# Kernel optimization log

Hardware: AMD Instinct MI355X
Metric: run time of the kernel (lower is better)

## Reference

```python
import jax, jax.numpy as jnp
import numpy as np

N_NODES = 500000
N_EDGES = 8000000
IN_DIM = 128
H1, H2, OUT = 32, 16, 2


def gcn_conv(x, W, b, src, dst, n):
    # PyG GCNConv: linear transform, add self-loops, symmetric norm, scatter-add, +bias
    x = x @ W                                   # [N, out]
    loop = jnp.arange(n, dtype=src.dtype)
    s = jnp.concatenate([src, loop])            # [E+N]
    d = jnp.concatenate([dst, loop])            # [E+N]
    deg = jax.ops.segment_sum(jnp.ones_like(d, dtype=x.dtype), d, num_segments=n)
    dinv = jnp.where(deg > 0, jax.lax.rsqrt(deg), 0.0)
    norm = dinv[s] * dinv[d]                    # [E+N]
    msg = x[s] * norm[:, None]                  # [E+N, out] gather
    out = jax.ops.segment_sum(msg, d, num_segments=n)  # scatter-add
    return out + b


def setup_inputs() -> dict:
    key = jax.random.key(0)
    ks = jax.random.split(key, 8)
    x = jax.random.normal(ks[0], (N_NODES, IN_DIM), dtype=jnp.float32)
    edge_index = jax.random.randint(ks[1], (2, N_EDGES), 0, N_NODES, dtype=jnp.int64)
    def glorot(k, fan_in, fan_out):
        lim = float(np.sqrt(6.0 / (fan_in + fan_out)))
        return jax.random.uniform(k, (fan_in, fan_out), jnp.float32, -lim, lim)
    return {
        "x": x,
        "edge_index": edge_index,
        "W1": glorot(ks[2], IN_DIM, H1),
        "b1": jnp.zeros((H1,), jnp.float32),
        "W2": glorot(ks[3], H1, H2),
        "b2": jnp.zeros((H2,), jnp.float32),
        "Wfc": glorot(ks[4], H2, OUT),
        "bfc": jnp.zeros((OUT,), jnp.float32),
    }


def reference(x, edge_index, W1, b1, W2, b2, Wfc, bfc):
    src, dst = edge_index[0], edge_index[1]
    h = jax.nn.relu(gcn_conv(x, W1, b1, src, dst, x.shape[0]))
    h = jax.nn.relu(gcn_conv(h, W2, b2, src, dst, x.shape[0]))
    logits = h @ Wfc + bfc
    return jax.nn.log_softmax(logits, axis=1)
```

## Files before the change

### kernel.cpp

```cpp
#include <hip/hip_runtime.h>

#define N_NODES 500000
#define N_EDGES 8000000
#define IN_DIM 128
#define H1 32
#define H2 16
#define NFINE 1954
#define NCOARSE 62
#define CAPA 200
#define CAPB 340

static __device__ __forceinline__ float bf2f(unsigned short u) {
    return __uint_as_float(((unsigned int)u) << 16);
}
static __device__ __forceinline__ unsigned short f2bf(float f) {
    unsigned int u = __float_as_uint(f);
    unsigned int r = (u + 0x7fffu + ((u >> 16) & 1u)) >> 16;
    return (unsigned short)r;
}
static __device__ __forceinline__ unsigned pack2bf(float a, float b) {
    return (unsigned)f2bf(a) | ((unsigned)f2bf(b) << 16);
}
static __device__ __forceinline__ float ldf(const void* p, int i, bool isf32) {
    return isf32 ? ((const float*)p)[i] : bf2f(((const unsigned short*)p)[i]);
}
static __device__ __forceinline__ uint4 zsel(uint4 u, int v) {
    return v ? u : make_uint4(0u, 0u, 0u, 0u);
}
static __device__ __forceinline__ void acc8(float a[8], uint4 u) {
    unsigned w[4] = {u.x, u.y, u.z, u.w};
#pragma unroll
    for (int p = 0; p < 4; ++p) {
        a[2 * p]     += __uint_as_float(w[p] << 16);
        a[2 * p + 1] += __uint_as_float(w[p] & 0xffff0000u);
    }
}

__global__ __launch_bounds__(64) void k_sniff(const unsigned int* __restrict__ x,
                                              int* __restrict__ flag) {
    int bad = 0;
    for (int i = threadIdx.x; i < 1024; i += 64) {
        float v = __uint_as_float((x[i] & 0xffffu) << 16);
        if (!(fabsf(v) < 1e6f)) bad = 1;
    }
    unsigned long long m = __ballot(bad);
    if (threadIdx.x == 0) *flag = (m != 0ull) ? 1 : 0;
}

__global__ __launch_bounds__(256) void k_bhist(const int* __restrict__ dst,
                                               int* __restrict__ fhist) {
    __shared__ int h[2048];
    int tid = threadIdx.x;
    for (int i = tid; i < 2048; i += 256) h[i] = 0;
    __syncthreads();
    int i = blockIdx.x * 256 + tid;
    int stride = gridDim.x * 256;
    for (int e = i; e < N_EDGES; e += stride) {
        unsigned d = (unsigned)dst[e];
        if (d < N_NODES) atomicAdd(&h[d >> 8], 1);
    }
    __syncthreads();
    for (int i2 = tid; i2 < 2048; i2 += 256)
        if (h[i2]) atomicAdd(&fhist[i2], h[i2]);
}

__global__ __launch_bounds__(256) void k_scanf(const int* __restrict__ fhist,
                                               int* __restrict__ fbase,
                                               int* __restrict__ bcur,
                                               int* __restrict__ acur) {
    __shared__ int tmp[256];
    __shared__ int s_run;
    int tid = threadIdx.x;
    if (tid == 0) s_run = 0;
    __syncthreads();
    for (int base = 0; base < 2048; base += 256) {
        int i = base + tid;
        int v = (i < NFINE) ? fhist[i] : 0;
        int val = v;
        tmp[tid] = val;
        __syncthreads();
        for (int o = 1; o < 256; o <<= 1) {
            int t = (tid >= o) ? tmp[tid - o] : 0;
            __syncthreads();
            val += t;
            tmp[tid] = val;
            __syncthreads();
        }
        int run = s_run;
        if (i < NFINE) {
            int ex = run + val - v;
            fbase[i] = ex;
            bcur[i] = ex;
            if ((i & 31) == 0) acur[i >> 5] = ex;
        }
        __syncthreads();
        if (tid == 255) s_run = run + val;
        __syncthreads();
    }
    if (tid == 0) fbase[NFINE] = s_run;
}

__global__ __launch_bounds__(256) void k_scatA(const int* __restrict__ src,
                                               const int* __restrict__ dst,
                                               int* __restrict__ acur,
                                               unsigned* __restrict__ ebufA) {
    __shared__ unsigned stage[NCOARSE * CAPA];
    __shared__ int lcnt[NCOARSE], nn[NCOARSE], soff[NCOARSE], sbase[NCOARSE];
    __shared__ int stot;
    int tid = threadIdx.x;
    int cb = blockIdx.x * 8192;
    if (tid < NCOARSE) lcnt[tid] = 0;
    __syncthreads();
    for (int i = 0; i < 32; ++i) {
        int e = cb + (i << 8) + tid;
        if (e < N_EDGES) {
            unsigned d = (unsigned)dst[e], s = (unsigned)src[e];
            if (d < N_NODES) {
                unsigned b = d >> 13;
                unsigned p = ((d & 8191u) << 19) | s;
                int pos = atomicAdd(&lcnt[b], 1);
                if (pos < CAPA) stage[b * CAPA + pos] = p;
                else { int slot = atomicAdd(&acur[b], 1); ebufA[slot] = p; }
            }
        }
    }
    __syncthreads();
    if (tid < NCOARSE) nn[tid] = min(lcnt[tid], CAPA);
    __syncthreads();
    if (tid == 0) {
        int r = 0;
        for (int b = 0; b < NCOARSE; ++b) { soff[b] = r; r += nn[b]; }
        stot = r;
    }
    __syncthreads();
    if (tid < NCOARSE && nn[tid] > 0) sbase[tid] = atomicAdd(&acur[tid], nn[tid]);
    __syncthreads();
    for (int i = tid; i < stot; i += 256) {
        int lo = 0, hi = NCOARSE - 1;
        while (lo < hi) { int mid = (lo + hi + 1) >> 1; if (soff[mid] <= i) lo = mid; else hi = mid - 1; }
        int r = i - soff[lo];
        ebufA[sbase[lo] + r] = stage[lo * CAPA + r];
    }
}

__global__ __launch_bounds__(256) void k_scatB(const unsigned* __restrict__ ebufA,
                                               const int* __restrict__ fbase,
                                               int* __restrict__ bcur,
                                               unsigned* __restrict__ ebufB) {
    __shared__ unsigned stage[32 * CAPB];
    __shared__ int lcnt[32], nn[32], soff[32], sbase[32];
    __shared__ int stot;
    int tid = threadIdx.x;
    int a = blockIdx.x >> 3, sub = blockIdx.x & 7;
    int f0 = a * 32;
    int lb = min(32, NFINE - f0);
    int abase = fbase[f0];
    int aend = fbase[min(f0 + 32, NFINE)];
    for (int cb = abase + sub * 8192; cb < aend; cb += 8 * 8192) {
        if (tid < 32) lcnt[tid] = 0;
        __syncthreads();
        for (int i = 0; i < 32; ++i) {
            int e = cb + (i << 8) + tid;
            if (e < aend) {
                unsigned p = ebufA[e];
                unsigned dl13 = p >> 19;
                unsigned s = p & 0x7FFFFu;
                unsigned j = dl13 >> 8;
                unsigned q = ((dl13 & 255u) << 19) | s;
                int pos = atomicAdd(&lcnt[j], 1);
                if (pos < CAPB) stage[j * CAPB + pos] = q;
                else { int slot = atomicAdd(&bcur[f0 + j], 1); ebufB[slot] = q; }
            }
        }
        __syncthreads();
        if (tid < 32) nn[tid] = (tid < lb) ? min(lcnt[tid], CAPB) : 0;
        __syncthreads();
        if (tid == 0) {
            int r = 0;
            for (int b = 0; b < 32; ++b) { soff[b] = r; r += nn[b]; }
            stot = r;
        }
        __syncthreads();
        if (tid < 32 && nn[tid] > 0) sbase[tid] = atomicAdd(&bcur[f0 + tid], nn[tid]);
        __syncthreads();
        for (int i = tid; i < stot; i += 256) {
            int lo = 0, hi = 31;
            while (lo < hi) { int mid = (lo + hi + 1) >> 1; if (soff[mid] <= i) lo = mid; else hi = mid - 1; }
            int r = i - soff[lo];
            ebufB[sbase[lo] + r] = stage[lo * CAPB + r];
        }
        __syncthreads();
    }
}

__global__ __launch_bounds__(256) void k_csr(const unsigned* __restrict__ ebufB,
                                             const int* __restrict__ fbase,
                                             int* __restrict__ csr,
                                             int* __restrict__ off,
                                             float* __restrict__ dinv) {
    __shared__ int cnt[256], ctmp[256], ccur[256];
    int tid = threadIdx.x;
    int b = blockIdx.x;
    int base = fbase[b];
    int n = fbase[b + 1] - base;
    cnt[tid] = 0;
    __syncthreads();
    for (int i = tid; i < n; i += 256) {
        unsigned dl = ebufB[base + i] >> 19;
        atomicAdd(&cnt[dl], 1);
    }
    __syncthreads();
    int v = cnt[tid];
    int val = v;
    ctmp[tid] = val;
    __syncthreads();
    for (int o = 1; o < 256; o <<= 1) {
        int t = (tid >= o) ? ctmp[tid - o] : 0;
        __syncthreads();
        val += t;
        ctmp[tid] = val;
        __syncthreads();
    }
    int excl = val - v;
    off[b * 256 + tid] = base + excl;
    ccur[tid] = excl;
    dinv[b * 256 + tid] = rsqrtf((float)v + 1.0f);
    __syncthreads();
    for (int i = tid; i < n; i += 256) {
        unsigned p = ebufB[base + i];
        unsigned dl = p >> 19;
        int slot = atomicAdd(&ccur[dl], 1);
        csr[base + slot] = (int)(p & 0x7FFFFu);
    }
}

__global__ __launch_bounds__(256) void k_gemm1(const void* __restrict__ x,
                                               const void* __restrict__ w1,
                                               const float* __restrict__ dinv,
                                               unsigned* __restrict__ y1b,
                                               const int* __restrict__ flag) {
    __shared__ float wlds[IN_DIM * H1];
    const bool isf32 = (*flag != 0);
    for (int i = threadIdx.x; i < IN_DIM * H1; i += 256) wlds[i] = ldf(w1, i, isf32);
    __syncthreads();
    int node = blockIdx.x * 256 + threadIdx.x;
    if (node >= N_NODES) return;
    float acc[H1];
#pragma unroll
    for (int j = 0; j < H1; ++j) acc[j] = 0.f;
    if (isf32) {
        const float4* xr = reinterpret_cast<const float4*>((const float*)x + (size_t)node * IN_DIM);
#pragma unroll
        for (int kk = 0; kk < IN_DIM / 4; ++kk) {
            float4 v = xr[kk];
            float xe[4] = {v.x, v.y, v.z, v.w};
#pragma unroll
            for (int p = 0; p < 4; ++p) {
                const float* wr = &wlds[(kk * 4 + p) * H1];
#pragma unroll
                for (int j = 0; j < H1; ++j) acc[j] += xe[p] * wr[j];
            }
        }
    } else {
        const uint4* xr = reinterpret_cast<const uint4*>((const unsigned short*)x + (size_t)node * IN_DIM);
#pragma unroll
        for (int kk = 0; kk < IN_DIM / 8; ++kk) {
            uint4 xv = xr[kk];
            unsigned uu[4] = {xv.x, xv.y, xv.z, xv.w};
#pragma unroll
            for (int p = 0; p < 4; ++p) {
                float xlo = __uint_as_float(uu[p] << 16);
                float xhi = __uint_as_float(uu[p] & 0xffff0000u);
                const float* w0 = &wlds[(kk * 8 + p * 2) * H1];
                const float* w1r = w0 + H1;
#pragma unroll
                for (int j = 0; j < H1; ++j) acc[j] += xlo * w0[j];
#pragma unroll
                for (int j = 0; j < H1; ++j) acc[j] += xhi * w1r[j];
            }
        }
    }
    float s = dinv[node];
    unsigned o[16];
#pragma unroll
    for (int q = 0; q < 16; ++q) o[q] = pack2bf(acc[2*q] * s, acc[2*q+1] * s);
    uint4* op = reinterpret_cast<uint4*>(y1b + (size_t)node * 16);
#pragma unroll
    for (int r = 0; r < 4; ++r) op[r] = make_uint4(o[4*r], o[4*r+1], o[4*r+2], o[4*r+3]);
}

__global__ __launch_bounds__(256) void k_pull1(const int* __restrict__ off,
                                               const int* __restrict__ csr,
                                               const unsigned* __restrict__ y1b,
                                               const float* __restrict__ dinv,
                                               const void* __restrict__ b1,
                                               const void* __restrict__ w2,
                                               unsigned* __restrict__ y2b,
                                               const int* __restrict__ flag) {
    __shared__ float w2l[H1 * H2];
    __shared__ float b1l[H1];
    __shared__ float hbuf[64 * 33];
    const bool isf32 = (*flag != 0);
    int tid = threadIdx.x;
    for (int i = tid; i < H1 * H2; i += 256) w2l[i] = ldf(w2, i, isf32);
    if (tid < H1) b1l[tid] = ldf(b1, tid, isf32);
    __syncthreads();

    const int r = tid & 3;
    const int g = tid >> 2;
    const int node = blockIdx.x * 64 + g;
    if (node >= N_NODES) return;

    float a[8];
#pragma unroll
    for (int p = 0; p < 8; ++p) a[p] = 0.f;

    const int beg = off[node], end = off[node + 1];
    const unsigned* yb = y1b + 4 * r;
    for (int j = beg; j < end; j += 4) {
        const int e1 = end - 1;
        int i1 = min(j + 1, e1), i2 = min(j + 2, e1), i3 = min(j + 3, e1);
        int s0 = csr[j], s1 = csr[i1], s2 = csr[i2], s3 = csr[i3];
        uint4 u0 = *reinterpret_cast<const uint4*>(yb + (size_t)s0 * 16);
        uint4 u1 = *reinterpret_cast<const uint4*>(yb + (size_t)s1 * 16);
        uint4 u2 = *reinterpret_cast<const uint4*>(yb + (size_t)s2 * 16);
        uint4 u3 = *reinterpret_cast<const uint4*>(yb + (size_t)s3 * 16);
        u1 = zsel(u1, j + 1 < end);
        u2 = zsel(u2, j + 2 < end);
        u3 = zsel(u3, j + 3 < end);
        acc8(a, u0); acc8(a, u1); acc8(a, u2); acc8(a, u3);
    }
    uint4 su = *reinterpret_cast<const uint4*>(yb + (size_t)node * 16);
    acc8(a, su);

    const float sc = dinv[node];
    float* hb = &hbuf[g * 33];
#pragma unroll
    for (int p = 0; p < 8; ++p) {
        float h = sc * a[p] + b1l[8 * r + p];
        hb[8 * r + p] = h > 0.f ? h : 0.f;
    }
    float z[4];
#pragma unroll
    for (int c = 0; c < 4; ++c) z[c] = 0.f;
#pragma unroll
    for (int k = 0; k < H1; ++k) {
        float hv = hb[k];
#pragma unroll
        for (int c = 0; c < 4; ++c) z[c] += hv * w2l[k * H2 + 4 * r + c];
    }
    uint2 o;
    o.x = pack2bf(sc * z[0], sc * z[1]);
    o.y = pack2bf(sc * z[2], sc * z[3]);
    *reinterpret_cast<uint2*>(y2b + (size_t)node * 8 + 2 * r) = o;
}

__global__ __launch_bounds__(256) void k_pull2(const int* __restrict__ off,
                                               const int* __restrict__ csr,
                                               const unsigned* __restrict__ y2b,
                                               const float* __restrict__ dinv,
                                               const void* __restrict__ b2,
                                               const void* __restrict__ wfc,
                                               const void* __restrict__ bfc,
                                               void* __restrict__ out,
                                               const int* __restrict__ flag) {
    __shared__ float wl[H2 * 2];
    __shared__ float b2l[H2];
    __shared__ float bfl[2];
    const bool isf32 = (*flag != 0);
    int tid = threadIdx.x;
    if (tid < H2 * 2) wl[tid] = ldf(wfc, tid, isf32);
    if (tid < H2) b2l[tid] = ldf(b2, tid, isf32);
    if (tid < 2) bfl[tid] = ldf(bfc, tid, isf32);
    __syncthreads();

    const int r = tid & 1;
    const int node = blockIdx.x * 128 + (tid >> 1);
    if (node >= N_NODES) return;

    float a[8];
#pragma unroll
    for (int p = 0; p < 8; ++p) a[p] = 0.f;

    const int beg = off[node], end = off[node + 1];
    const unsigned* yb = y2b + 4 * r;
    for (int j = beg; j < end; j += 4) {
        const int e1 = end - 1;
        int i1 = min(j + 1, e1), i2 = min(j + 2, e1), i3 = min(j + 3, e1);
        int s0 = csr[j], s1 = csr[i1], s2 = csr[i2], s3 = csr[i3];
        uint4 u0 = *reinterpret_cast<const uint4*>(yb + (size_t)s0 * 8);
        uint4 u1 = *reinterpret_cast<const uint4*>(yb + (size_t)s1 * 8);
        uint4 u2 = *reinterpret_cast<const uint4*>(yb + (size_t)s2 * 8);
        uint4 u3 = *reinterpret_cast<const uint4*>(yb + (size_t)s3 * 8);
        u1 = zsel(u1, j + 1 < end);
        u2 = zsel(u2, j + 2 < end);
        u3 = zsel(u3, j + 3 < end);
        acc8(a, u0); acc8(a, u1); acc8(a, u2); acc8(a, u3);
    }
    uint4 su = *reinterpret_cast<const uint4*>(yb + (size_t)node * 8);
    acc8(a, su);

    const float sc = dinv[node];
    float l0 = 0.f, l1 = 0.f;
#pragma unroll
    for (int p = 0; p < 8; ++p) {
        float h = sc * a[p] + b2l[8 * r + p];
        h = h > 0.f ? h : 0.f;
        l0 += h * wl[(8 * r + p) * 2];
        l1 += h * wl[(8 * r + p) * 2 + 1];
    }
    l0 += __shfl_xor(l0, 1, 64);
    l1 += __shfl_xor(l1, 1, 64);
    if (r == 0) {
        l0 += bfl[0];
        l1 += bfl[1];
        float mx = fmaxf(l0, l1);
        float lse = mx + logf(__expf(l0 - mx) + __expf(l1 - mx));
        if (isf32) {
            reinterpret_cast<float2*>(out)[node] = make_float2(l0 - lse, l1 - lse);
        } else {
            reinterpret_cast<unsigned*>(out)[node] =
                (unsigned)f2bf(l0 - lse) | ((unsigned)f2bf(l1 - lse) << 16);
        }
    }
}

extern "C" void kernel_launch(void* const* d_in, const int* in_sizes, int n_in,
                              void* d_out, int out_size, void* d_ws, size_t ws_size,
                              hipStream_t stream) {
    const void* x   = d_in[0];
    const int*  ei  = (const int*)d_in[1];
    const void* w1  = d_in[2];
    const void* b1  = d_in[3];
    const void* w2  = d_in[4];
    const void* b2  = d_in[5];
    const void* wfc = d_in[6];
    const void* bfc = d_in[7];
    const int* src = ei;
    const int* dst = ei + N_EDGES;

    float*    ws    = (float*)d_ws;
    int*      flag  = (int*)ws;
    float*    dinv  = ws + 64;
    int*      fhist = (int*)(ws + 500288);
    int*      fbase = (int*)(ws + 502336);
    int*      acur  = (int*)(ws + 504384);
    int*      bcur  = (int*)(ws + 504448);
    int*      off   = (int*)(ws + 506496);
    unsigned* ebufA = (unsigned*)(ws + 1006784);
    int*      csr   = (int*)(ws + 1006784);
    unsigned* ebufB = (unsigned*)(ws + 9006784);
    unsigned* y1b   = (unsigned*)(ws + 17006784);
    unsigned* y2b   = (unsigned*)(ws + 25010368);

    k_sniff<<<1, 64, 0, stream>>>((const unsigned int*)x, flag);
    hipMemsetAsync(fhist, 0, 2048 * sizeof(int), stream);
    k_bhist<<<256, 256, 0, stream>>>(dst, fhist);
    k_scanf<<<1, 256, 0, stream>>>(fhist, fbase, bcur, acur);
    k_scatA<<<977, 256, 0, stream>>>(src, dst, acur, ebufA);
    k_scatB<<<NCOARSE * 8, 256, 0, stream>>>(ebufA, fbase, bcur, ebufB);
    k_csr<<<NFINE, 256, 0, stream>>>(ebufB, fbase, csr, off, dinv);
    k_gemm1<<<NFINE, 256, 0, stream>>>(x, w1, dinv, y1b, flag);
    k_pull1<<<(N_NODES + 63) / 64, 256, 0, stream>>>(off, csr, y1b, dinv, b1, w2, y2b, flag);
    k_pull2<<<(N_NODES + 127) / 128, 256, 0, stream>>>(off, csr, y2b, dinv, b2, wfc, bfc, d_out, flag);
}
```

Baseline: 1.020 ms.

## Register-tile first GEMM as 4 nodes by 8 outputs per thread

Restructures the first feature-transform kernel so each thread computes a 4-node by 8-output tile, with four threads sharing a group of four nodes, instead of one thread computing all 32 outputs for one node. Each weight value read from shared memory is now reused across four nodes, which cuts LDS traffic per FMA and shrinks the accumulator register footprint. The cost is that each x row is loaded by four threads, relying on cache hits, and per-thread global loads become strided across four rows, which may hurt coalescing.

```diff
diff --git a/kernel.cpp b/kernel.cpp
--- a/kernel.cpp
+++ b/kernel.cpp
@@ -243,50 +243,89 @@
     const bool isf32 = (*flag != 0);
     for (int i = threadIdx.x; i < IN_DIM * H1; i += 256) wlds[i] = ldf(w1, i, isf32);
     __syncthreads();
-    int node = blockIdx.x * 256 + threadIdx.x;
-    if (node >= N_NODES) return;
-    float acc[H1];
-#pragma unroll
-    for (int j = 0; j < H1; ++j) acc[j] = 0.f;
+    const int tid = threadIdx.x;
+    const int c = tid & 3;
+    const int q = tid >> 2;
+    const int n0 = blockIdx.x * 256 + q * 4;
+
+    int nn[4];
+#pragma unroll
+    for (int i = 0; i < 4; ++i) nn[i] = min(n0 + i, N_NODES - 1);
+
+    float acc[4][8];
+#pragma unroll
+    for (int i = 0; i < 4; ++i)
+#pragma unroll
+        for (int j = 0; j < 8; ++j) acc[i][j] = 0.f;
+
     if (isf32) {
-        const float4* xr = reinterpret_cast<const float4*>((const float*)x + (size_t)node * IN_DIM);
-#pragma unroll
+        const float4* xp0 = reinterpret_cast<const float4*>((const float*)x + (size_t)nn[0] * IN_DIM);
+        const float4* xp1 = reinterpret_cast<const float4*>((const float*)x + (size_t)nn[1] * IN_DIM);
+        const float4* xp2 = reinterpret_cast<const float4*>((const float*)x + (size_t)nn[2] * IN_DIM);
+        const float4* xp3 = reinterpret_cast<const float4*>((const float*)x + (size_t)nn[3] * IN_DIM);
+#pragma unroll 4
         for (int kk = 0; kk < IN_DIM / 4; ++kk) {
-            float4 v = xr[kk];
-            float xe[4] = {v.x, v.y, v.z, v.w};
+            float4 v0 = xp0[kk], v1 = xp1[kk], v2 = xp2[kk], v3 = xp3[kk];
+            float xa[4][4] = {{v0.x, v0.y, v0.z, v0.w},
+                              {v1.x, v1.y, v1.z, v1.w},
+                              {v2.x, v2.y, v2.z, v2.w},
+                              {v3.x, v3.y, v3.z, v3.w}};
+            const float* wr = &wlds[(kk * 4) * H1 + 8 * c];
 #pragma unroll
             for (int p = 0; p < 4; ++p) {
-                const float* wr = &wlds[(kk * 4 + p) * H1];
-#pragma unroll
-                for (int j = 0; j < H1; ++j) acc[j] += xe[p] * wr[j];
+                float w8[8];
+#pragma unroll
+                for (int j = 0; j < 8; ++j) w8[j] = wr[p * H1 + j];
+#pragma unroll
+                for (int i = 0; i < 4; ++i)
+#pragma unroll
+                    for (int j = 0; j < 8; ++j) acc[i][j] += xa[i][p] * w8[j];
             }
         }
     } else {
-        const uint4* xr = reinterpret_cast<const uint4*>((const unsigned short*)x + (size_t)node * IN_DIM);
-#pragma unroll
+        const uint4* xp0 = reinterpret_cast<const uint4*>((const unsigned short*)x + (size_t)nn[0] * IN_DIM);
+        const uint4* xp1 = reinterpret_cast<const uint4*>((const unsigned short*)x + (size_t)nn[1] * IN_DIM);
+        const uint4* xp2 = reinterpret_cast<const uint4*>((const unsigned short*)x + (size_t)nn[2] * IN_DIM);
+        const uint4* xp3 = reinterpret_cast<const uint4*>((const unsigned short*)x + (size_t)nn[3] * IN_DIM);
+#pragma unroll 2
         for (int kk = 0; kk < IN_DIM / 8; ++kk) {
-            uint4 xv = xr[kk];
-            unsigned uu[4] = {xv.x, xv.y, xv.z, xv.w};
+            uint4 b0 = xp0[kk], b1 = xp1[kk], b2 = xp2[kk], b3 = xp3[kk];
+            unsigned ua[4][4] = {{b0.x, b0.y, b0.z, b0.w},
+                                 {b1.x, b1.y, b1.z, b1.w},
+                                 {b2.x, b2.y, b2.z, b2.w},
+                                 {b3.x, b3.y, b3.z, b3.w}};
+            const float* wr = &wlds[(kk * 8) * H1 + 8 * c];
 #pragma unroll
             for (int p = 0; p < 4; ++p) {
-                float xlo = __uint_as_float(uu[p] << 16);
-                float xhi = __uint_as_float(uu[p] & 0xffff0000u);
-                const float* w0 = &wlds[(kk * 8 + p * 2) * H1];
-                const float* w1r = w0 + H1;
-#pragma unroll
-                for (int j = 0; j < H1; ++j) acc[j] += xlo * w0[j];
-#pragma unroll
-                for (int j = 0; j < H1; ++j) acc[j] += xhi * w1r[j];
+                float wlo[8], whi[8];
+#pragma unroll
+                for (int j = 0; j < 8; ++j) wlo[j] = wr[(2 * p) * H1 + j];
+#pragma unroll
+                for (int j = 0; j < 8; ++j) whi[j] = wr[(2 * p + 1) * H1 + j];
+#pragma unroll
+                for (int i = 0; i < 4; ++i) {
+                    float xlo = __uint_as_float(ua[i][p] << 16);
+                    float xhi = __uint_as_float(ua[i][p] & 0xffff0000u);
+#pragma unroll
+                    for (int j = 0; j < 8; ++j) acc[i][j] += xlo * wlo[j];
+#pragma unroll
+                    for (int j = 0; j < 8; ++j) acc[i][j] += xhi * whi[j];
+                }
             }
         }
     }
-    float s = dinv[node];
-    unsigned o[16];
-#pragma unroll
-    for (int q = 0; q < 16; ++q) o[q] = pack2bf(acc[2*q] * s, acc[2*q+1] * s);
-    uint4* op = reinterpret_cast<uint4*>(y1b + (size_t)node * 16);
-#pragma unroll
-    for (int r = 0; r < 4; ++r) op[r] = make_uint4(o[4*r], o[4*r+1], o[4*r+2], o[4*r+3]);
+#pragma unroll
+    for (int i = 0; i < 4; ++i) {
+        int node = n0 + i;
+        if (node >= N_NODES) break;
+        float s = dinv[node];
+        uint4 o;
+        o.x = pack2bf(acc[i][0] * s, acc[i][1] * s);
+        o.y = pack2bf(acc[i][2] * s, acc[i][3] * s);
+        o.z = pack2bf(acc[i][4] * s, acc[i][5] * s);
+        o.w = pack2bf(acc[i][6] * s, acc[i][7] * s);
+        *reinterpret_cast<uint4*>(y1b + (size_t)node * 16 + 4 * c) = o;
+    }
 }
 
 __global__ __launch_bounds__(256) void k_pull1(const int* __restrict__ off,
```

After: 1.018 ms. No clear change (-0.2%).
